# Kernel optimization log

Hardware: AMD Instinct MI355X
Metric: run time of the kernel (lower is better)

## Reference

```python
import jax, jax.numpy as jnp
import numpy as np

N_NODES = 100000
N_EDGES = 800000
D_IN = 128
D_HID = 128
D_OUT = 128
NUM_GRAPHS = 64


def gcn_conv(x, src, dst, W, b, n_nodes):
    """PyG GCNConv: h = D^{-1/2} (A + I) D^{-1/2} (x W) + b, with self-loops included in src/dst."""
    h = x @ W  # [N, d_out]
    deg = jax.ops.segment_sum(jnp.ones_like(dst, dtype=h.dtype), dst, num_segments=n_nodes)
    dinv = jnp.where(deg > 0, jax.lax.rsqrt(deg), 0.0)
    norm = dinv[src] * dinv[dst]  # [E]
    out = jax.ops.segment_sum(h[src] * norm[:, None], dst, num_segments=n_nodes)
    return out + b


def setup_inputs() -> dict:
    key = jax.random.key(0)
    ks = jax.random.split(key, 10)
    x = jax.random.normal(ks[0], (N_NODES, D_IN), dtype=jnp.float32)
    edge_index = jax.random.randint(ks[1], (2, N_EDGES), 0, N_NODES, dtype=jnp.int64)
    batch = jnp.sort(jax.random.randint(ks[2], (N_NODES,), 0, NUM_GRAPHS, dtype=jnp.int64))
    s1 = 1.0 / np.sqrt(D_IN)
    s2 = 1.0 / np.sqrt(D_HID)
    W1 = jax.random.uniform(ks[3], (D_IN, D_HID), jnp.float32, -s1, s1)
    b1 = jnp.zeros((D_HID,), jnp.float32)
    W2 = jax.random.uniform(ks[4], (D_HID, D_HID), jnp.float32, -s2, s2)
    b2 = jnp.zeros((D_HID,), jnp.float32)
    Wfc = jax.random.uniform(ks[5], (D_HID, D_OUT), jnp.float32, -s2, s2)
    bfc = jax.random.uniform(ks[6], (D_OUT,), jnp.float32, -s2, s2)
    return {"x": x, "edge_index": edge_index, "batch": batch,
            "W1": W1, "b1": b1, "W2": W2, "b2": b2, "Wfc": Wfc, "bfc": bfc}


def reference(x, edge_index, batch, W1, b1, W2, b2, Wfc, bfc):
    n = x.shape[0]
    loop = jnp.arange(n, dtype=edge_index.dtype)
    src = jnp.concatenate([edge_index[0], loop])
    dst = jnp.concatenate([edge_index[1], loop])
    h = jax.nn.relu(gcn_conv(x, src, dst, W1, b1, n))
    h = jax.nn.relu(gcn_conv(h, src, dst, W2, b2, n))
    # global_mean_pool over graph ids
    sums = jax.ops.segment_sum(h, batch, num_segments=NUM_GRAPHS)
    cnts = jax.ops.segment_sum(jnp.ones((n,), h.dtype), batch, num_segments=NUM_GRAPHS)
    pooled = sums / jnp.maximum(cnts, 1.0)[:, None]
    return pooled @ Wfc + bfc
```

## Files before the change

### kernel.cpp

```cpp
#include <hip/hip_runtime.h>
#include <hip/hip_bf16.h>

#define N_NODES 100000
#define N_EDGES 800000
#define D 128
#define NG 64
#define SCAN_NB ((N_NODES + 255) / 256)
#define NTILES ((N_NODES + 63) / 64)

typedef __attribute__((ext_vector_type(8))) short short8;
typedef __attribute__((ext_vector_type(4))) float f32x4;
typedef __attribute__((ext_vector_type(2))) float f32x2;

static __device__ __forceinline__ unsigned short f2bf(float f) {
    unsigned u = __float_as_uint(f);
    unsigned r = (u + 0x7FFF + ((u >> 16) & 1)) >> 16;
    return (unsigned short)r;
}
static __device__ __forceinline__ float bf2f(unsigned short b) {
    return __uint_as_float((unsigned)b << 16);
}
static __device__ __forceinline__ unsigned char f2fp8(float v) {
    int p = __builtin_amdgcn_cvt_pk_fp8_f32(v, v, 0, false);
    return (unsigned char)(p & 0xFF);
}


__global__ void hist_kernel(const int* __restrict__ dst, int* __restrict__ deg) {
    int e = blockIdx.x * blockDim.x + threadIdx.x;
    if (e < N_EDGES) atomicAdd(&deg[dst[e]], 1);
}

__global__ __launch_bounds__(256) void scan1_kernel(const int* __restrict__ deg,
                                                    int* __restrict__ rs,
                                                    int* __restrict__ bsum,
                                                    float* __restrict__ dinv) {
    __shared__ int wsum[4];
    int i = blockIdx.x * 256 + threadIdx.x;
    int lane = threadIdx.x & 63;
    int wid = threadIdx.x >> 6;
    int v = (i < N_NODES) ? deg[i] : 0;
    if (i < N_NODES) dinv[i] = rsqrtf((float)v + 1.0f);
    int x = v;
    #pragma unroll
    for (int off = 1; off < 64; off <<= 1) {
        int y = __shfl_up(x, off);
        if (lane >= off) x += y;
    }
    if (lane == 63) wsum[wid] = x;
    __syncthreads();
    int add = 0;
    #pragma unroll
    for (int w = 0; w < 3; ++w) if (w < wid) add += wsum[w];
    int incl = x + add;
    if (i < N_NODES) rs[i + 1] = incl - v;
    if (threadIdx.x == 255) bsum[blockIdx.x] = incl;
}

__global__ __launch_bounds__(512) void scan2_kernel(int* __restrict__ bsum) {
    __shared__ int s[512];
    int t = threadIdx.x;
    int v = (t < SCAN_NB) ? bsum[t] : 0;
    s[t] = v;
    __syncthreads();
    for (int off = 1; off < 512; off <<= 1) {
        int y = (t >= off) ? s[t - off] : 0;
        __syncthreads();
        s[t] += y;
        __syncthreads();
    }
    if (t < SCAN_NB) bsum[t] = s[t] - v;
}

__global__ void scan3_kernel(int* __restrict__ rs, const int* __restrict__ bsum) {
    int i = blockIdx.x * blockDim.x + threadIdx.x;
    if (i < N_NODES) rs[i + 1] += bsum[i >> 8];
    if (i == 0) rs[0] = 0;
}

__global__ void fill_kernel(const int* __restrict__ src, const int* __restrict__ dst,
                            int* __restrict__ rs, int* __restrict__ pairs) {
    int e = blockIdx.x * blockDim.x + threadIdx.x;
    if (e < N_EDGES) {
        int d = dst[e];
        int p = atomicAdd(&rs[1 + d], 1);
        pairs[p] = src[e];
    }
}


__global__ void bounds_kernel(const int* __restrict__ batch, int* __restrict__ start,
                              unsigned int* __restrict__ sentinel) {
    int g = threadIdx.x;
    if (g < 32) sentinel[g] = 0u;
    if (g > NG) return;
    if (g == NG) { start[NG] = N_NODES; return; }
    int lo = 0, hi = N_NODES;
    while (lo < hi) {
        int mid = (lo + hi) >> 1;
        if (batch[mid] < g) lo = mid + 1; else hi = mid;
    }
    start[g] = lo;
}


template <bool IN_F32>
__global__ __launch_bounds__(512) void xw_mfma_kernel(const void* __restrict__ Xin,
                                                      const float* __restrict__ W,
                                                      const float* __restrict__ dinv,
                                                      unsigned char* __restrict__ Hq) {
    __shared__ __align__(16) unsigned short bt_hi[128 * 128];
    __shared__ __align__(16) unsigned short bt_lo[128 * 128];
    __shared__ __align__(16) unsigned short atile[64 * 128];

    const int t = threadIdx.x;
    const int lane = t & 63;
    const int wid = t >> 6;

    #pragma unroll 4
    for (int i = 0; i < 32; ++i) {
        int idx = t + i * 512;
        int k = idx >> 7;
        int n = idx & 127;
        float w = W[idx];
        unsigned short hi = f2bf(w);
        unsigned short lo = f2bf(w - bf2f(hi));
        int byte = (n * 256 + k * 2) ^ ((n & 7) << 4);
        *(unsigned short*)((char*)bt_hi + byte) = hi;
        *(unsigned short*)((char*)bt_lo + byte) = lo;
    }

    const int mrow = (wid >> 1) * 16;
    const int ncol = (wid & 1) * 64;
    const int ar = mrow + (lane & 15);
    const int ak = (lane >> 4) * 8;

    for (int tile = blockIdx.x; tile < NTILES; tile += gridDim.x) {
        const int node0 = tile * 64;
        __syncthreads();

        #pragma unroll
        for (int p = 0; p < 2; ++p) {
            int j = t + p * 512;
            int row = j >> 4;
            int c8 = (j & 15) * 8;
            int node = node0 + row;
            short8 v = 0;
            if (IN_F32) {
                const float* X = (const float*)Xin;
                if (node < N_NODES) {
                    const float* xr = &X[(size_t)node * 128 + c8];
                    float4 a = *(const float4*)xr;
                    float4 b = *(const float4*)(xr + 4);
                    v[0] = (short)f2bf(a.x); v[1] = (short)f2bf(a.y);
                    v[2] = (short)f2bf(a.z); v[3] = (short)f2bf(a.w);
                    v[4] = (short)f2bf(b.x); v[5] = (short)f2bf(b.y);
                    v[6] = (short)f2bf(b.z); v[7] = (short)f2bf(b.w);
                }
            } else {
                const unsigned short* X = (const unsigned short*)Xin;
                if (node < N_NODES) v = *(const short8*)&X[(size_t)node * 128 + c8];
            }
            int byte = (row * 256 + c8 * 2) ^ ((row & 7) << 4);
            *(short8*)((char*)atile + byte) = v;
        }
        __syncthreads();

        f32x4 acc[4];
        #pragma unroll
        for (int nt = 0; nt < 4; ++nt) acc[nt] = 0.f;

        #pragma unroll
        for (int kc = 0; kc < 128; kc += 32) {
            short8 a = *(const short8*)((const char*)atile +
                        ((ar * 256 + (kc + ak) * 2) ^ ((ar & 7) << 4)));
            #pragma unroll
            for (int nt = 0; nt < 4; ++nt) {
                int col = ncol + nt * 16 + (lane & 15);
                int boff = (col * 256 + (kc + ak) * 2) ^ ((col & 7) << 4);
                short8 bh = *(const short8*)((const char*)bt_hi + boff);
                acc[nt] = __builtin_amdgcn_mfma_f32_16x16x32_bf16(a, bh, acc[nt], 0, 0, 0);
                short8 bl = *(const short8*)((const char*)bt_lo + boff);
                acc[nt] = __builtin_amdgcn_mfma_f32_16x16x32_bf16(a, bl, acc[nt], 0, 0, 0);
            }
        }

        #pragma unroll
        for (int r = 0; r < 4; ++r) {
            int node = node0 + mrow + (lane >> 4) * 4 + r;
            if (node < N_NODES) {
                float di = dinv[node];
                #pragma unroll
                for (int nt = 0; nt < 4; ++nt)
                    Hq[(size_t)node * 128 + ncol + nt * 16 + (lane & 15)] = f2fp8(acc[nt][r] * di);
            }
        }
    }
}


#define ACC8ADD(HV)                                                        \
    {                                                                      \
        f32x2 _h0 = __builtin_amdgcn_cvt_pk_f32_fp8((int)(HV).x, false);   \
        f32x2 _h1 = __builtin_amdgcn_cvt_pk_f32_fp8((int)(HV).x, true);    \
        f32x2 _h2 = __builtin_amdgcn_cvt_pk_f32_fp8((int)(HV).y, false);   \
        f32x2 _h3 = __builtin_amdgcn_cvt_pk_f32_fp8((int)(HV).y, true);    \
        acc[0] += _h0[0]; acc[1] += _h0[1];                                \
        acc[2] += _h1[0]; acc[3] += _h1[1];                                \
        acc[4] += _h2[0]; acc[5] += _h2[1];                                \
        acc[6] += _h3[0]; acc[7] += _h3[1];                                \
    }

__global__ __launch_bounds__(256) void gather_kernel(const unsigned char* __restrict__ Hq,
                                                     const int* __restrict__ rs,
                                                     const int* __restrict__ pairs,
                                                     const float* __restrict__ dinv,
                                                     const float* __restrict__ bias,
                                                     unsigned short* __restrict__ out) {
    int node = blockIdx.x * 4 + (threadIdx.x >> 6);
    if (node >= N_NODES) return;
    const int lane = threadIdx.x & 63;
    const int g = lane >> 4;
    const int fl = lane & 15;

    int beg = rs[node];
    int end = rs[node + 1];
    int deg = end - beg;

    float acc[8];
    if (g == 0) {
        uint2 sv = *(const uint2*)&Hq[(size_t)node * 128 + fl * 8];
        f32x2 a0 = __builtin_amdgcn_cvt_pk_f32_fp8((int)sv.x, false);
        f32x2 a1 = __builtin_amdgcn_cvt_pk_f32_fp8((int)sv.x, true);
        f32x2 a2 = __builtin_amdgcn_cvt_pk_f32_fp8((int)sv.y, false);
        f32x2 a3 = __builtin_amdgcn_cvt_pk_f32_fp8((int)sv.y, true);
        acc[0] = a0[0]; acc[1] = a0[1];
        acc[2] = a1[0]; acc[3] = a1[1];
        acc[4] = a2[0]; acc[5] = a2[1];
        acc[6] = a3[0]; acc[7] = a3[1];
    } else {
        #pragma unroll
        for (int j = 0; j < 8; ++j) acc[j] = 0.f;
    }

    if (deg > 0) {
        int pall = pairs[beg + min(lane, deg - 1)];
        int niter = (deg + 3) >> 2;

        const int j0 = g, j1 = g + 4, j2 = g + 8, j3 = g + 12;
        int s0 = (j0 < deg) ? __shfl(pall, j0) : N_NODES;
        int s1 = (j1 < deg) ? __shfl(pall, j1) : N_NODES;
        int s2 = (j2 < deg) ? __shfl(pall, j2) : N_NODES;
        int s3 = (j3 < deg) ? __shfl(pall, j3) : N_NODES;

        uint2 h0 = make_uint2(0u, 0u), h1 = h0, h2 = h0, h3 = h0;
        h0 = *(const uint2*)&Hq[(size_t)s0 * 128 + fl * 8];
        if (niter > 1) h1 = *(const uint2*)&Hq[(size_t)s1 * 128 + fl * 8];
        if (niter > 2) h2 = *(const uint2*)&Hq[(size_t)s2 * 128 + fl * 8];
        if (niter > 3) h3 = *(const uint2*)&Hq[(size_t)s3 * 128 + fl * 8];

        ACC8ADD(h0);
        ACC8ADD(h1);
        ACC8ADD(h2);
        ACC8ADD(h3);

        if (deg > 16) {
            for (int j = 16 + g; j < deg; j += 4) {
                int s = pairs[beg + j];
                uint2 hv = *(const uint2*)&Hq[(size_t)s * 128 + fl * 8];
                ACC8ADD(hv);
            }
        }
    }

    #pragma unroll
    for (int mask = 16; mask <= 32; mask <<= 1) {
        #pragma unroll
        for (int j = 0; j < 8; ++j) acc[j] += __shfl_xor(acc[j], mask);
    }

    if (g == 0) {
        float di = dinv[node];
        float4 bb0 = *(const float4*)&bias[fl * 8];
        float4 bb1 = *(const float4*)&bias[fl * 8 + 4];
        short8 o;
        o[0] = (short)f2bf(fmaxf(fmaf(acc[0], di, bb0.x), 0.f));
        o[1] = (short)f2bf(fmaxf(fmaf(acc[1], di, bb0.y), 0.f));
        o[2] = (short)f2bf(fmaxf(fmaf(acc[2], di, bb0.z), 0.f));
        o[3] = (short)f2bf(fmaxf(fmaf(acc[3], di, bb0.w), 0.f));
        o[4] = (short)f2bf(fmaxf(fmaf(acc[4], di, bb1.x), 0.f));
        o[5] = (short)f2bf(fmaxf(fmaf(acc[5], di, bb1.y), 0.f));
        o[6] = (short)f2bf(fmaxf(fmaf(acc[6], di, bb1.z), 0.f));
        o[7] = (short)f2bf(fmaxf(fmaf(acc[7], di, bb1.w), 0.f));
        *(short8*)&out[(size_t)node * 128 + fl * 8] = o;
    }
}


__global__ __launch_bounds__(256) void pool_kernel(const unsigned short* __restrict__ G,
                                                   const int* __restrict__ start,
                                                   float* __restrict__ sums) {
    __shared__ float red[16][132];
    int g = blockIdx.x >> 4;
    int s = blockIdx.x & 15;
    int n0 = start[g], n1 = start[g + 1];
    int slot = threadIdx.x & 15;
    int nl = threadIdx.x >> 4;

    float acc[8];
    #pragma unroll
    for (int j = 0; j < 8; ++j) acc[j] = 0.f;

    for (int node = n0 + s * 16 + nl; node < n1; node += 256) {
        short8 v = *(const short8*)&G[(size_t)node * 128 + slot * 8];
        #pragma unroll
        for (int j = 0; j < 8; ++j) acc[j] += bf2f((unsigned short)v[j]);
    }

    #pragma unroll
    for (int j = 0; j < 8; ++j) red[nl][slot * 8 + j] = acc[j];
    __syncthreads();
    #pragma unroll
    for (int off = 8; off > 0; off >>= 1) {
        if (nl < off) {
            #pragma unroll
            for (int j = 0; j < 8; ++j)
                red[nl][slot * 8 + j] += red[nl + off][slot * 8 + j];
        }
        __syncthreads();
    }
    if (nl == 0) {
        #pragma unroll
        for (int j = 0; j < 8; ++j)
            unsafeAtomicAdd(&sums[g * D + slot * 8 + j], red[0][slot * 8 + j]);
    }
}


__global__ void fc_kernel(const float* __restrict__ sums, const int* __restrict__ start,
                          const float* __restrict__ Wfc, const float* __restrict__ bfc,
                          float* __restrict__ out) {
    __shared__ __align__(16) float ps[D];
    int g = blockIdx.x;
    int f = threadIdx.x;
    float c = (float)max(start[g + 1] - start[g], 1);
    ps[f] = sums[g * D + f] / c;
    __syncthreads();
    float acc = bfc[f];
    #pragma unroll
    for (int k = 0; k < D; k += 4) {
        float4 pv = *(const float4*)&ps[k];
        acc += pv.x * Wfc[k * D + f] + pv.y * Wfc[(k + 1) * D + f] +
               pv.z * Wfc[(k + 2) * D + f] + pv.w * Wfc[(k + 3) * D + f];
    }
    out[g * D + f] = acc;
}

extern "C" void kernel_launch(void* const* d_in, const int* in_sizes, int n_in,
                              void* d_out, int out_size, void* d_ws, size_t ws_size,
                              hipStream_t stream) {
    const float* x   = (const float*)d_in[0];
    const int* ei    = (const int*)d_in[1];
    const int* batch = (const int*)d_in[2];
    const float* W1  = (const float*)d_in[3];
    const float* b1  = (const float*)d_in[4];
    const float* W2  = (const float*)d_in[5];
    const float* b2  = (const float*)d_in[6];
    const float* Wfc = (const float*)d_in[7];
    const float* bfc = (const float*)d_in[8];
    float* out = (float*)d_out;

    const int* src = ei;
    const int* dst = ei + N_EDGES;

    unsigned char* Hq    = (unsigned char*)d_ws;
    unsigned short* G    = (unsigned short*)(Hq + (size_t)(N_NODES + 1) * D);
    int* pairs           = (int*)(G + (size_t)N_NODES * D);
    float* dinv          = (float*)(pairs + N_EDGES);
    int*   deg           = (int*)(dinv + N_NODES);
    int*   rs            = deg + N_NODES;
    int*   bsum          = rs + N_NODES + 4;
    int*   start         = bsum + 512;
    float* sums          = (float*)(start + NG + 8);

    hipMemsetAsync(deg, 0, N_NODES * sizeof(int), stream);
    hipMemsetAsync(sums, 0, NG * D * sizeof(float), stream);

    hist_kernel<<<(N_EDGES + 255) / 256, 256, 0, stream>>>(dst, deg);
    scan1_kernel<<<SCAN_NB, 256, 0, stream>>>(deg, rs, bsum, dinv);
    scan2_kernel<<<1, 512, 0, stream>>>(bsum);
    scan3_kernel<<<SCAN_NB, 256, 0, stream>>>(rs, bsum);
    fill_kernel<<<(N_EDGES + 255) / 256, 256, 0, stream>>>(src, dst, rs, pairs);
    bounds_kernel<<<1, 128, 0, stream>>>(batch, start,
                                         (unsigned int*)(Hq + (size_t)N_NODES * D));

    xw_mfma_kernel<true><<<512, 512, 0, stream>>>(x, W1, dinv, Hq);
    gather_kernel<<<(N_NODES + 3) / 4, 256, 0, stream>>>(Hq, rs, pairs, dinv, b1, G);

    xw_mfma_kernel<false><<<512, 512, 0, stream>>>(G, W2, dinv, Hq);
    gather_kernel<<<(N_NODES + 3) / 4, 256, 0, stream>>>(Hq, rs, pairs, dinv, b2, G);

    pool_kernel<<<NG * 16, 256, 0, stream>>>(G, start, sums);
    fc_kernel<<<NG, 128, 0, stream>>>(sums, start, Wfc, bfc, out);
}
```

Baseline: 314.2 us.

## Fuse scan stages, bounds search, CSR fill into fewer launches; drop pool atomics

Merges the block-sum scan and its offset application into one multi-block kernel, with each block redundantly rescanning the block sums. The graph-bounds binary search and sentinel clear move into that kernel, and the CSR fill moves into the first X·W MFMA kernel. The pool kernel now writes per-block partial sums that the FC kernel reduces, which removes the atomics and the sums memset. Together these cut about four launches and their gaps, at the cost of redundant scan work per block and atomic fill traffic competing with the GEMM. Gather also skips accumulating unused slots.

```diff
diff --git a/kernel.cpp b/kernel.cpp
--- a/kernel.cpp
+++ b/kernel.cpp
@@ -57,7 +57,11 @@
     if (threadIdx.x == 255) bsum[blockIdx.x] = incl;
 }
 
-__global__ __launch_bounds__(512) void scan2_kernel(int* __restrict__ bsum) {
+__global__ __launch_bounds__(512) void scan23_kernel(int* __restrict__ rs,
+                                                     const int* __restrict__ bsum,
+                                                     const int* __restrict__ batch,
+                                                     int* __restrict__ start,
+                                                     unsigned int* __restrict__ sentinel) {
     __shared__ int s[512];
     int t = threadIdx.x;
     int v = (t < SCAN_NB) ? bsum[t] : 0;
@@ -69,46 +73,40 @@
         s[t] += y;
         __syncthreads();
     }
-    if (t < SCAN_NB) bsum[t] = s[t] - v;
-}
-
-__global__ void scan3_kernel(int* __restrict__ rs, const int* __restrict__ bsum) {
-    int i = blockIdx.x * blockDim.x + threadIdx.x;
-    if (i < N_NODES) rs[i + 1] += bsum[i >> 8];
+    int i = blockIdx.x * 512 + t;
+    if (i < N_NODES) {
+        int c = i >> 8;
+        rs[i + 1] += s[c] - bsum[c];
+    }
     if (i == 0) rs[0] = 0;
-}
-
-__global__ void fill_kernel(const int* __restrict__ src, const int* __restrict__ dst,
-                            int* __restrict__ rs, int* __restrict__ pairs) {
-    int e = blockIdx.x * blockDim.x + threadIdx.x;
-    if (e < N_EDGES) {
-        int d = dst[e];
-        int p = atomicAdd(&rs[1 + d], 1);
-        pairs[p] = src[e];
-    }
-}
-
-
-__global__ void bounds_kernel(const int* __restrict__ batch, int* __restrict__ start,
-                              unsigned int* __restrict__ sentinel) {
-    int g = threadIdx.x;
-    if (g < 32) sentinel[g] = 0u;
-    if (g > NG) return;
-    if (g == NG) { start[NG] = N_NODES; return; }
-    int lo = 0, hi = N_NODES;
-    while (lo < hi) {
-        int mid = (lo + hi) >> 1;
-        if (batch[mid] < g) lo = mid + 1; else hi = mid;
-    }
-    start[g] = lo;
-}
-
-
-template <bool IN_F32>
+
+    if (blockIdx.x == 0) {
+        if (t < 32) sentinel[t] = 0u;
+        if (t >= 64 && t <= 64 + NG) {
+            int g = t - 64;
+            if (g == NG) { start[NG] = N_NODES; }
+            else {
+                int lo = 0, hi = N_NODES;
+                while (lo < hi) {
+                    int mid = (lo + hi) >> 1;
+                    if (batch[mid] < g) lo = mid + 1; else hi = mid;
+                }
+                start[g] = lo;
+            }
+        }
+    }
+}
+
+
+template <bool IN_F32, bool DO_FILL>
 __global__ __launch_bounds__(512) void xw_mfma_kernel(const void* __restrict__ Xin,
                                                       const float* __restrict__ W,
                                                       const float* __restrict__ dinv,
-                                                      unsigned char* __restrict__ Hq) {
+                                                      unsigned char* __restrict__ Hq,
+                                                      const int* __restrict__ src,
+                                                      const int* __restrict__ dst,
+                                                      int* __restrict__ rs,
+                                                      int* __restrict__ pairs) {
     __shared__ __align__(16) unsigned short bt_hi[128 * 128];
     __shared__ __align__(16) unsigned short bt_lo[128 * 128];
     __shared__ __align__(16) unsigned short atile[64 * 128];
@@ -116,6 +114,19 @@
     const int t = threadIdx.x;
     const int lane = t & 63;
     const int wid = t >> 6;
+
+    if (DO_FILL) {
+        int tg = blockIdx.x * 512 + t;
+        #pragma unroll
+        for (int i = 0; i < 4; ++i) {
+            int e = tg + i * 262144;
+            if (e < N_EDGES) {
+                int d = dst[e];
+                int p = atomicAdd(&rs[1 + d], 1);
+                pairs[p] = src[e];
+            }
+        }
+    }
 
     #pragma unroll 4
     for (int i = 0; i < 32; ++i) {
@@ -253,16 +264,16 @@
         int s2 = (j2 < deg) ? __shfl(pall, j2) : N_NODES;
         int s3 = (j3 < deg) ? __shfl(pall, j3) : N_NODES;
 
-        uint2 h0 = make_uint2(0u, 0u), h1 = h0, h2 = h0, h3 = h0;
+        uint2 h0, h1, h2, h3;
         h0 = *(const uint2*)&Hq[(size_t)s0 * 128 + fl * 8];
         if (niter > 1) h1 = *(const uint2*)&Hq[(size_t)s1 * 128 + fl * 8];
         if (niter > 2) h2 = *(const uint2*)&Hq[(size_t)s2 * 128 + fl * 8];
         if (niter > 3) h3 = *(const uint2*)&Hq[(size_t)s3 * 128 + fl * 8];
 
         ACC8ADD(h0);
-        ACC8ADD(h1);
-        ACC8ADD(h2);
-        ACC8ADD(h3);
+        if (niter > 1) ACC8ADD(h1);
+        if (niter > 2) ACC8ADD(h2);
+        if (niter > 3) ACC8ADD(h3);
 
         if (deg > 16) {
             for (int j = 16 + g; j < deg; j += 4) {
@@ -299,7 +310,7 @@
 
 __global__ __launch_bounds__(256) void pool_kernel(const unsigned short* __restrict__ G,
                                                    const int* __restrict__ start,
-                                                   float* __restrict__ sums) {
+                                                   float* __restrict__ partial) {
     __shared__ float red[16][132];
     int g = blockIdx.x >> 4;
     int s = blockIdx.x & 15;
@@ -330,21 +341,24 @@
         __syncthreads();
     }
     if (nl == 0) {
-        #pragma unroll
-        for (int j = 0; j < 8; ++j)
-            unsafeAtomicAdd(&sums[g * D + slot * 8 + j], red[0][slot * 8 + j]);
-    }
-}
-
-
-__global__ void fc_kernel(const float* __restrict__ sums, const int* __restrict__ start,
+        float* prow = &partial[(size_t)blockIdx.x * D + slot * 8];
+        *(float4*)&prow[0] = *(const float4*)&red[0][slot * 8];
+        *(float4*)&prow[4] = *(const float4*)&red[0][slot * 8 + 4];
+    }
+}
+
+
+__global__ void fc_kernel(const float* __restrict__ partial, const int* __restrict__ start,
                           const float* __restrict__ Wfc, const float* __restrict__ bfc,
                           float* __restrict__ out) {
     __shared__ __align__(16) float ps[D];
     int g = blockIdx.x;
     int f = threadIdx.x;
     float c = (float)max(start[g + 1] - start[g], 1);
-    ps[f] = sums[g * D + f] / c;
+    float accp = 0.f;
+    #pragma unroll
+    for (int s = 0; s < 16; ++s) accp += partial[(size_t)(g * 16 + s) * D + f];
+    ps[f] = accp / c;
     __syncthreads();
     float acc = bfc[f];
     #pragma unroll
@@ -381,25 +395,21 @@
     int*   rs            = deg + N_NODES;
     int*   bsum          = rs + N_NODES + 4;
     int*   start         = bsum + 512;
-    float* sums          = (float*)(start + NG + 8);
+    float* partial       = (float*)(start + NG + 8);
 
     hipMemsetAsync(deg, 0, N_NODES * sizeof(int), stream);
-    hipMemsetAsync(sums, 0, NG * D * sizeof(float), stream);
 
     hist_kernel<<<(N_EDGES + 255) / 256, 256, 0, stream>>>(dst, deg);
     scan1_kernel<<<SCAN_NB, 256, 0, stream>>>(deg, rs, bsum, dinv);
-    scan2_kernel<<<1, 512, 0, stream>>>(bsum);
-    scan3_kernel<<<SCAN_NB, 256, 0, stream>>>(rs, bsum);
-    fill_kernel<<<(N_EDGES + 255) / 256, 256, 0, stream>>>(src, dst, rs, pairs);
-    bounds_kernel<<<1, 128, 0, stream>>>(batch, start,
-                                         (unsigned int*)(Hq + (size_t)N_NODES * D));
-
-    xw_mfma_kernel<true><<<512, 512, 0, stream>>>(x, W1, dinv, Hq);
+    scan23_kernel<<<(N_NODES + 511) / 512, 512, 0, stream>>>(
+        rs, bsum, batch, start, (unsigned int*)(Hq + (size_t)N_NODES * D));
+
+    xw_mfma_kernel<true, true><<<512, 512, 0, stream>>>(x, W1, dinv, Hq, src, dst, rs, pairs);
     gather_kernel<<<(N_NODES + 3) / 4, 256, 0, stream>>>(Hq, rs, pairs, dinv, b1, G);
 
-    xw_mfma_kernel<false><<<512, 512, 0, stream>>>(G, W2, dinv, Hq);
+    xw_mfma_kernel<false, false><<<512, 512, 0, stream>>>(G, W2, dinv, Hq, src, dst, rs, pairs);
     gather_kernel<<<(N_NODES + 3) / 4, 256, 0, stream>>>(Hq, rs, pairs, dinv, b2, G);
 
-    pool_kernel<<<NG * 16, 256, 0, stream>>>(G, start, sums);
-    fc_kernel<<<NG, 128, 0, stream>>>(sums, start, Wfc, bfc, out);
-}
+    pool_kernel<<<NG * 16, 256, 0, stream>>>(G, start, partial);
+    fc_kernel<<<NG, 128, 0, stream>>>(partial, start, Wfc, bfc, out);
+}
```

Measured after the change: 303.2 us. -3.5%, faster.
